# Optimization experiments

Hardware: AMD Instinct MI355X
Metric: run time of the kernel (lower is better)

Reference implementation:

```python
import jax, jax.numpy as jnp
import numpy as np

EPS = 1e-3  # tfa GroupNormalization default epsilon


def setup_inputs() -> dict:
    key = jax.random.key(0)
    ks = jax.random.split(key, 6)
    B, H, W, C = 8, 64, 64, 256
    x = jax.random.normal(ks[0], (B, H, W, C), dtype=jnp.float32)
    s = 0.05  # keep activations in a numerically sane range
    return {
        "x": x,
        "gamma": jnp.ones((C,), jnp.float32),
        "beta": jnp.zeros((C,), jnp.float32),
        "wq": jax.random.normal(ks[1], (C, C), jnp.float32) * s,
        "bq": jnp.zeros((C,), jnp.float32),
        "wk": jax.random.normal(ks[2], (C, C), jnp.float32) * s,
        "bk": jnp.zeros((C,), jnp.float32),
        "wv": jax.random.normal(ks[3], (C, C), jnp.float32) * s,
        "bv": jnp.zeros((C,), jnp.float32),
        "wp": jax.random.normal(ks[4], (C, C), jnp.float32) * s,
        "bp": jnp.zeros((C,), jnp.float32),
    }


def _group_norm1(x, gamma, beta):
    # GroupNorm with 1 group: normalize over (H, W, C) per sample,
    # per-channel affine. tfa default epsilon=1e-3.
    mean = jnp.mean(x, axis=(1, 2, 3), keepdims=True)
    var = jnp.var(x, axis=(1, 2, 3), keepdims=True)
    return (x - mean) * jax.lax.rsqrt(var + EPS) * gamma + beta


def reference(x, gamma, beta, wq, bq, wk, bk, wv, bv, wp, bp):
    B, H, W, C = x.shape
    h = _group_norm1(x, gamma, beta)
    hf = h.reshape(B, H * W, C)  # flatten spatial -> tokens
    q = hf @ wq + bq
    k = hf @ wk + bk
    v = hf @ wv + bv
    scale = jnp.float32(C) ** -0.5
    # full [B, N, N] attention scores, N = H*W (faithful to the einsum)
    scores = jnp.einsum('bnc,bmc->bnm', q, k) * scale
    attn = jax.nn.softmax(scores, axis=-1)
    o = jnp.einsum('bnm,bmc->bnc', attn, v)
    o = o @ wp + bp
    return x + o.reshape(B, H, W, C)
```

## Files before the change

### kernel.cpp

```cpp
#include <hip/hip_runtime.h>
#include <hip/hip_bf16.h>

typedef __attribute__((ext_vector_type(8))) short short8;
typedef __attribute__((ext_vector_type(4))) float f32x4;
typedef __attribute__((ext_vector_type(16))) float f32x16;
typedef long long ll_t;

#define WS_PART 0u
#define WS_WT 8192u
#define WS_ML 532480u
#define WS_Q  2097152u
#define WS_K  (WS_Q + 16777216u)
#define WS_V  (WS_K + 16777216u)
#define WS_VT (WS_V + 16777216u)
#define WS_O  (WS_VT + 16777216u)

#define SM_C2 4.3280851f

__device__ __forceinline__ unsigned short f2bf(float f) {
  unsigned int u = __builtin_bit_cast(unsigned int, f);
  u += 0x7fffu + ((u >> 16) & 1u);
  return (unsigned short)(u >> 16);
}
__device__ __forceinline__ float bf2f(unsigned short h) {
  unsigned int u = ((unsigned int)h) << 16;
  return __builtin_bit_cast(float, u);
}
__device__ __forceinline__ unsigned char f2fp8(float f) {
  return (unsigned char)(__builtin_amdgcn_cvt_pk_fp8_f32(f, f, 0, false) & 0xff);
}

__device__ __forceinline__ void gl_lds16(const unsigned short* g, unsigned short* l) {
  __builtin_amdgcn_global_load_lds(
      (const __attribute__((address_space(1))) unsigned int*)g,
      (__attribute__((address_space(3))) unsigned int*)l, 16, 0, 0);
}

__device__ __forceinline__ f32x4 mfma_fp8(ll_t a, ll_t b, f32x4 c) {
  return __builtin_amdgcn_mfma_f32_16x16x32_fp8_fp8(a, b, c, 0, 0, 0);
}

__global__ void k_wt(const float* __restrict__ wq, const float* __restrict__ wk,
                     const float* __restrict__ wv, const float* __restrict__ wp,
                     unsigned short* __restrict__ wT) {
  int m = blockIdx.x >> 8;
  int c = blockIdx.x & 255;
  const float* w = (m == 0) ? wq : (m == 1) ? wk : (m == 2) ? wv : wp;
  int d = threadIdx.x;
  wT[(size_t)(m * 256 + d) * 256 + c] = f2bf(w[c * 256 + d]);
}

__global__ void k_gn_part(const float* __restrict__ x, float2* __restrict__ part) {
  int b = blockIdx.x >> 5, seg = blockIdx.x & 31;
  const float4* xp = (const float4*)(x + ((size_t)b << 20) + ((size_t)seg << 15));
  float s = 0.f, sq = 0.f;
  for (int i = 0; i < 32; ++i) {
    float4 v = xp[threadIdx.x + i * 256];
    s += v.x + v.y + v.z + v.w;
    sq += v.x * v.x + v.y * v.y + v.z * v.z + v.w * v.w;
  }
  for (int m = 1; m <= 32; m <<= 1) { s += __shfl_xor(s, m); sq += __shfl_xor(sq, m); }
  __shared__ float2 red[4];
  int w = threadIdx.x >> 6;
  if ((threadIdx.x & 63) == 0) red[w] = make_float2(s, sq);
  __syncthreads();
  if (threadIdx.x == 0) {
    float S = 0.f, Q = 0.f;
    for (int i = 0; i < 4; ++i) { S += red[i].x; Q += red[i].y; }
    part[blockIdx.x] = make_float2(S, Q);
  }
}

__global__ __launch_bounds__(256) void k_qkv(
    const float* __restrict__ x, const float* __restrict__ gamma, const float* __restrict__ beta,
    const float* __restrict__ bq, const float* __restrict__ bk, const float* __restrict__ bv,
    const float2* __restrict__ part, const unsigned short* __restrict__ wT,
    unsigned char* __restrict__ q8, unsigned char* __restrict__ k8,
    unsigned char* __restrict__ vt8)
{
  __shared__ unsigned short SMEM[16384];
  __shared__ float2 stSh;
  unsigned short* const As = SMEM;
  unsigned short* const Bs = SMEM + 8192;
  const int bm = blockIdx.x, bn = blockIdx.y;
  const int mat = bn >> 1, dbase = (bn & 1) * 128;
  const int tid = threadIdx.x, lane = tid & 63, w = tid >> 6;
  const int wm = w >> 1, wn = w & 1;
  const int m0 = bm * 128;
  if (tid < 32) {
    float2 p = part[(bm >> 5) * 32 + tid];
    float s = p.x, sq = p.y;
    for (int m = 1; m <= 16; m <<= 1) { s += __shfl_xor(s, m); sq += __shfl_xor(sq, m); }
    if (tid == 0) {
      float mean = s * (1.f / 1048576.f);
      float var = sq * (1.f / 1048576.f) - mean * mean;
      stSh = make_float2(mean, rsqrtf(var + 1e-3f));
    }
  }
  __syncthreads();
  const float2 st = stSh;
  f32x16 acc[2][2] = {};
  for (int ks = 0; ks < 4; ++ks) {
    for (int i = 0; i < 8; ++i) {
      int chunk = tid + i * 256;
      int row = chunk >> 4, cq = (chunk & 15) * 4;
      int c = ks * 64 + cq;
      const float4 xv = *(const float4*)(x + (size_t)(m0 + row) * 256 + c);
      const float4 g = *(const float4*)(gamma + c);
      const float4 bt = *(const float4*)(beta + c);
      unsigned short h[4];
      h[0] = f2bf((xv.x - st.x) * st.y * g.x + bt.x);
      h[1] = f2bf((xv.y - st.x) * st.y * g.y + bt.y);
      h[2] = f2bf((xv.z - st.x) * st.y * g.z + bt.z);
      h[3] = f2bf((xv.w - st.x) * st.y * g.w + bt.w);
      *(uint2*)(&As[row * 64 + (cq ^ ((row & 7) << 3))]) = *(uint2*)h;
    }
    for (int i = 0; i < 4; ++i) {
      int chunk = tid + i * 256;
      int row = chunk >> 3, cc = (chunk & 7) * 8;
      const uint4* src = (const uint4*)(wT + (size_t)(mat * 256 + dbase + row) * 256 + ks * 64 + cc);
      *(uint4*)(&Bs[row * 64 + (cc ^ ((row & 7) << 3))]) = *src;
    }
    __syncthreads();
    for (int kk = 0; kk < 4; ++kk) {
      short8 a[2], b[2];
      for (int mi = 0; mi < 2; ++mi) {
        int row = wm * 64 + mi * 32 + (lane & 31);
        int off = (kk * 16 + (lane >> 5) * 8) ^ ((row & 7) << 3);
        a[mi] = *(const short8*)(&As[row * 64 + off]);
      }
      for (int ni = 0; ni < 2; ++ni) {
        int row = wn * 64 + ni * 32 + (lane & 31);
        int off = (kk * 16 + (lane >> 5) * 8) ^ ((row & 7) << 3);
        b[ni] = *(const short8*)(&Bs[row * 64 + off]);
      }
      for (int mi = 0; mi < 2; ++mi)
        for (int ni = 0; ni < 2; ++ni)
          acc[mi][ni] = __builtin_amdgcn_mfma_f32_32x32x16_bf16(a[mi], b[ni], acc[mi][ni], 0, 0, 0);
    }
    __syncthreads();
  }
  const int batch = bm >> 5;
  if (mat == 0) {
    const float qs = 0.25f * 1.44269504f;
    for (int ni = 0; ni < 2; ++ni) {
      int dcol = dbase + wn * 64 + ni * 32 + (lane & 31);
      float bv_ = bq[dcol];
      for (int mi = 0; mi < 2; ++mi)
        for (int r = 0; r < 16; ++r) {
          int rowD = (r & 3) + 8 * (r >> 2) + 4 * (lane >> 5);
          int token = m0 + wm * 64 + mi * 32 + rowD;
          q8[(size_t)token * 256 + dcol] = f2fp8((acc[mi][ni][r] + bv_) * qs);
        }
    }
  } else if (mat == 1) {
    for (int ni = 0; ni < 2; ++ni) {
      int dcol = dbase + wn * 64 + ni * 32 + (lane & 31);
      float bv_ = bk[dcol];
      size_t cbase = (size_t)(batch * 32 + (dcol >> 3)) * 32768 + (dcol & 7);
      for (int mi = 0; mi < 2; ++mi)
        for (int r = 0; r < 16; ++r) {
          int rowD = (r & 3) + 8 * (r >> 2) + 4 * (lane >> 5);
          int token = (m0 + wm * 64 + mi * 32 + rowD) & 4095;
          k8[cbase + (size_t)token * 8] = f2fp8((acc[mi][ni][r] + bv_) * 0.25f);
        }
    }
  } else {
    unsigned char* SB = (unsigned char*)SMEM;
    for (int ni = 0; ni < 2; ++ni) {
      int dloc = wn * 64 + ni * 32 + (lane & 31);
      float bv_ = bv[dbase + dloc];
      for (int mi = 0; mi < 2; ++mi)
        for (int r = 0; r < 16; ++r) {
          int tloc = wm * 64 + mi * 32 + (r & 3) + 8 * (r >> 2) + 4 * (lane >> 5);
          SB[dloc * 128 + (tloc ^ ((dloc & 7) << 4))] = f2fp8(acc[mi][ni][r] + bv_);
        }
    }
    __syncthreads();
    const int Tbase = (bm & 31) * 16;
    for (int i2 = 0; i2 < 4; ++i2) {
      int u = tid + i2 * 256;
      int T = u >> 6;
      int dp = u & 63;
      int d0 = dp * 2;
      int tb = T * 8;
      uint2 lo = *(const uint2*)(&SB[d0 * 128 + (tb ^ ((d0 & 7) << 4))]);
      uint2 hi2 = *(const uint2*)(&SB[(d0 + 1) * 128 + (tb ^ (((d0 + 1) & 7) << 4))]);
      uint4 vv = { lo.x, lo.y, hi2.x, hi2.y };
      *(uint4*)(vt8 + ((size_t)(batch * 512 + Tbase + T) * 256 + dbase + d0) * 8) = vv;
    }
  }
}

__global__ __launch_bounds__(512, 4) void k_attn(
    const unsigned char* __restrict__ q8, const unsigned char* __restrict__ k8,
    const unsigned char* __restrict__ vt8,
    unsigned short* __restrict__ part0, unsigned short* __restrict__ part1,
    float* __restrict__ lsum)
{
  __shared__ unsigned char LDSb[65536];
  unsigned char* const Ks0 = LDSb;
  unsigned char* const Ks1 = LDSb + 16384;
  unsigned char* const Vt0 = LDSb + 32768;
  unsigned char* const Vt1 = LDSb + 49152;
  const int g = blockIdx.x & 15, qt = blockIdx.x >> 4;
  const int batch = g >> 1, half = g & 1;
  const int q0 = qt * 128;
  const int tid = threadIdx.x, lane = tid & 63, li = lane & 15, hi = lane >> 4, w = tid >> 6;

  ll_t qf8[8];
  {
    const size_t qtok = (size_t)(batch * 4096 + q0 + w * 16 + li);
#pragma unroll
    for (int kt = 0; kt < 8; ++kt)
      qf8[kt] = *(const ll_t*)(q8 + qtok * 256 + kt * 32 + hi * 8);
  }
  f32x4 acc[16] = {};
  float l_r = 0.f;
  const int idx0 = ((((hi << 1) + 0) & 3) * 16 + li) << 2;
  const int idx1 = ((((hi << 1) + 1) & 3) * 16 + li) << 2;

  unsigned kSrc[2];
  int kDst[2], vOff[2];
#pragma unroll
  for (int i = 0; i < 2; ++i) {
    kSrc[i] = (unsigned)((w * 4 + 2 * i + (lane >> 5)) * 32768 + (lane & 31) * 16);
    kDst[i] = (w * 4 + 2 * i) * 512 + lane * 16;
    vOff[i] = w * 2048 + i * 1024 + lane * 16;
  }
  const unsigned char* kb = k8 + (size_t)batch * 1048576 + half * 16384;
  const unsigned char* vb = vt8 + (size_t)batch * 1048576 + half * 524288;

#define STAGE(KD, VD) do {                                              \
    _Pragma("unroll")                                                   \
    for (int i = 0; i < 2; ++i)                                         \
      gl_lds16((const unsigned short*)(kb + kSrc[i]),                   \
               (unsigned short*)(KD + kDst[i]));                        \
    _Pragma("unroll")                                                   \
    for (int i = 0; i < 2; ++i)                                         \
      gl_lds16((const unsigned short*)(vb + vOff[i]),                   \
               (unsigned short*)(VD + vOff[i]));                        \
  } while (0)

#define QK(KVF, SDST, KC) do {                                               \
    _Pragma("unroll")                                                        \
    for (int ct = 0; ct < 2; ++ct)                                           \
      _Pragma("unroll")                                                      \
      for (int kt = 0; kt < 8; ++kt) {                                       \
        int boff = (((kt * 4 + hi) * 64) + (KVF) * 32 + ct * 16 + li) * 8;   \
        ll_t kf = *(const ll_t*)(&KC[boff]);                                 \
        SDST[ct] = mfma_fp8(kf, qf8[kt], SDST[ct]);                          \
      }                                                                      \
  } while (0)

#define SOFTMAX(SARR, PF) do {                                               \
    _Pragma("unroll")                                                        \
    for (int ct = 0; ct < 2; ++ct)                                           \
      _Pragma("unroll")                                                      \
      for (int r = 0; r < 4; ++r) {                                          \
        float p = exp2f(SARR[ct][r] - SM_C2);                                \
        SARR[ct][r] = p;                                                     \
        l_r += p;                                                            \
      }                                                                      \
    int D0 = __builtin_amdgcn_cvt_pk_fp8_f32(SARR[0][0], SARR[0][1], 0, false); \
    D0 = __builtin_amdgcn_cvt_pk_fp8_f32(SARR[0][2], SARR[0][3], D0, true);     \
    int D1 = __builtin_amdgcn_cvt_pk_fp8_f32(SARR[1][0], SARR[1][1], 0, false); \
    D1 = __builtin_amdgcn_cvt_pk_fp8_f32(SARR[1][2], SARR[1][3], D1, true);     \
    int a0 = __builtin_amdgcn_ds_bpermute(idx0, D0);                         \
    int a1 = __builtin_amdgcn_ds_bpermute(idx0, D1);                         \
    int b0 = __builtin_amdgcn_ds_bpermute(idx1, D0);                         \
    int b1 = __builtin_amdgcn_ds_bpermute(idx1, D1);                         \
    bool sel = (lane & 32) != 0;                                             \
    int2 pw = { sel ? a1 : a0, sel ? b1 : b0 };                              \
    PF = __builtin_bit_cast(ll_t, pw);                                       \
  } while (0)

#define PV(KVF, PF, VC) do {                                                 \
    __builtin_amdgcn_s_setprio(1);                                          \
    _Pragma("unroll")                                                        \
    for (int dt = 0; dt < 16; ++dt) {                                        \
      int boff = ((((KVF) * 4 + hi) * 256) + dt * 16 + li) * 8;              \
      ll_t vf = *(const ll_t*)(&VC[boff]);                                   \
      acc[dt] = mfma_fp8(PF, vf, acc[dt]);                                   \
    }                                                                        \
    __builtin_amdgcn_s_setprio(0);                                          \
  } while (0)

  STAGE(Ks0, Vt0);
  for (int it = 0; it < 32; ++it) {
    const int cur = it & 1;
    __syncthreads();
    if (it < 31) {
      kb += 512;
      vb += 16384;
      if (cur) STAGE(Ks0, Vt0); else STAGE(Ks1, Vt1);
    }
    const unsigned char* Kc = cur ? Ks1 : Ks0;
    const unsigned char* Vc = cur ? Vt1 : Vt0;

    {
      f32x4 s0[2] = {};
      __builtin_amdgcn_s_setprio(1);
      QK(0, s0, Kc);
      __builtin_amdgcn_s_setprio(0);
      ll_t pf0;
      SOFTMAX(s0, pf0);
      PV(0, pf0, Vc);
    }
    {
      f32x4 s1[2] = {};
      __builtin_amdgcn_s_setprio(1);
      QK(1, s1, Kc);
      __builtin_amdgcn_s_setprio(0);
      ll_t pf1;
      SOFTMAX(s1, pf1);
      PV(1, pf1, Vc);
    }
  }
#undef STAGE
#undef QK
#undef SOFTMAX
#undef PV
  l_r += __shfl_xor(l_r, 16);
  l_r += __shfl_xor(l_r, 32);
  __syncthreads();
  if (lane < 16)
    lsum[half * 32768 + (size_t)batch * 4096 + q0 + w * 16 + lane] = l_r;
  unsigned short* Lw = (unsigned short*)LDSb + w * 4096;
#pragma unroll
  for (int dt = 0; dt < 16; ++dt)
#pragma unroll
    for (int r = 0; r < 4; ++r)
      Lw[(hi * 4 + r) * 256 + dt * 16 + li] = f2bf(acc[dt][r]);
  unsigned short* pout = (half ? part1 : part0) + ((size_t)batch * 4096 + q0 + w * 16) * 256;
#pragma unroll
  for (int i = 0; i < 8; ++i) {
    short8 v = *(const short8*)(&Lw[i * 512 + lane * 8]);
    int row = i * 2 + (lane >> 5);
    *(short8*)(pout + row * 256 + (lane & 31) * 8) = v;
  }
}

__global__ __launch_bounds__(256) void k_proj(
    const unsigned short* __restrict__ p0, const unsigned short* __restrict__ p1,
    const float* __restrict__ lsum, const unsigned short* __restrict__ wT,
    const float* __restrict__ bp, const float* __restrict__ x, float* __restrict__ out)
{
  __shared__ unsigned short As[128 * 64];
  __shared__ unsigned short Bs[128 * 64];
  const int bm = blockIdx.x, bn = blockIdx.y;
  const int dbase = bn * 128;
  const int tid = threadIdx.x, lane = tid & 63, w = tid >> 6;
  const int wm = w >> 1, wn = w & 1;
  const int m0 = bm * 128;
  f32x16 acc[2][2] = {};
  for (int ks = 0; ks < 4; ++ks) {
    for (int i = 0; i < 4; ++i) {
      int chunk = tid + i * 256;
      int row = chunk >> 3, cc = (chunk & 7) * 8;
      int tok = m0 + row;
      float r = 1.f / (lsum[tok] + lsum[32768 + tok]);
      short8 u0 = *(const short8*)(p0 + (size_t)tok * 256 + ks * 64 + cc);
      short8 u1 = *(const short8*)(p1 + (size_t)tok * 256 + ks * 64 + cc);
      unsigned short hh[8];
      for (int j = 0; j < 8; ++j)
        hh[j] = f2bf(r * (bf2f((unsigned short)u0[j]) + bf2f((unsigned short)u1[j])));
      *(uint4*)(&As[row * 64 + (cc ^ ((row & 7) << 3))]) = *(uint4*)hh;
    }
    for (int i = 0; i < 4; ++i) {
      int chunk = tid + i * 256;
      int row = chunk >> 3, cc = (chunk & 7) * 8;
      const uint4* src = (const uint4*)(wT + (size_t)(3 * 256 + dbase + row) * 256 + ks * 64 + cc);
      *(uint4*)(&Bs[row * 64 + (cc ^ ((row & 7) << 3))]) = *src;
    }
    __syncthreads();
    for (int kk = 0; kk < 4; ++kk) {
      short8 a[2], b[2];
      for (int mi = 0; mi < 2; ++mi) {
        int row = wm * 64 + mi * 32 + (lane & 31);
        int off = (kk * 16 + (lane >> 5) * 8) ^ ((row & 7) << 3);
        a[mi] = *(const short8*)(&As[row * 64 + off]);
      }
      for (int ni = 0; ni < 2; ++ni) {
        int row = wn * 64 + ni * 32 + (lane & 31);
        int off = (kk * 16 + (lane >> 5) * 8) ^ ((row & 7) << 3);
        b[ni] = *(const short8*)(&Bs[row * 64 + off]);
      }
      for (int mi = 0; mi < 2; ++mi)
        for (int ni = 0; ni < 2; ++ni)
          acc[mi][ni] = __builtin_amdgcn_mfma_f32_32x32x16_bf16(a[mi], b[ni], acc[mi][ni], 0, 0, 0);
    }
    __syncthreads();
  }
  for (int ni = 0; ni < 2; ++ni) {
    int dcol = dbase + wn * 64 + ni * 32 + (lane & 31);
    float bv_ = bp[dcol];
    for (int mi = 0; mi < 2; ++mi)
      for (int r = 0; r < 16; ++r) {
        int rowD = (r & 3) + 8 * (r >> 2) + 4 * (lane >> 5);
        size_t idx = (size_t)(m0 + wm * 64 + mi * 32 + rowD) * 256 + dcol;
        out[idx] = x[idx] + acc[mi][ni][r] + bv_;
      }
  }
}

extern "C" void kernel_launch(void* const* d_in, const int* in_sizes, int n_in,
                              void* d_out, int out_size, void* d_ws, size_t ws_size,
                              hipStream_t stream) {
  const float* x = (const float*)d_in[0];
  const float* gamma = (const float*)d_in[1];
  const float* beta = (const float*)d_in[2];
  const float* wq = (const float*)d_in[3];
  const float* bq = (const float*)d_in[4];
  const float* wk = (const float*)d_in[5];
  const float* bk = (const float*)d_in[6];
  const float* wv = (const float*)d_in[7];
  const float* bv = (const float*)d_in[8];
  const float* wp = (const float*)d_in[9];
  const float* bp = (const float*)d_in[10];
  char* ws = (char*)d_ws;
  float2* part = (float2*)(ws + WS_PART);
  unsigned short* wT = (unsigned short*)(ws + WS_WT);
  float* lsw = (float*)(ws + WS_ML);
  unsigned char* q8 = (unsigned char*)(ws + WS_Q);
  unsigned char* k8 = (unsigned char*)(ws + WS_K);
  unsigned short* vw = (unsigned short*)(ws + WS_V);
  unsigned char* vt8 = (unsigned char*)(ws + WS_VT);
  unsigned short* ow = (unsigned short*)(ws + WS_O);
  float* out = (float*)d_out;

  k_wt<<<1024, 256, 0, stream>>>(wq, wk, wv, wp, wT);
  k_gn_part<<<256, 256, 0, stream>>>(x, part);
  k_qkv<<<dim3(256, 6), 256, 0, stream>>>(x, gamma, beta, bq, bk, bv, part, wT, q8, k8, vt8);
  k_attn<<<512, 512, 0, stream>>>(q8, k8, vt8, vw, ow, lsw);
  k_proj<<<dim3(256, 2), 256, 0, stream>>>(vw, ow, lsw, wT, bp, x, out);
}
```

Before: 182.0 us.

## Merge weight transpose with GN stats; compute all QKV outputs per token tile

The weight-transpose kernel and the group-norm partial-sum kernel are merged into a single launch with block-index dispatch, removing one kernel launch. The QKV kernel is restructured so each 512-thread block normalizes a 64-token tile once into LDS and then loops over Q, K and V and both output halves. Before, each block recomputed the normalized activations for only one of six output slices, so x was read and normalized six times. The cost is more serialized per-block work, more barriers and smaller MFMA tiles per wave, which lowers parallelism (512 blocks instead of 1536).

After: 177.6 us. 1.02x faster.

```diff
diff --git a/kernel.cpp b/kernel.cpp
--- a/kernel.cpp
+++ b/kernel.cpp
@@ -40,18 +40,21 @@
   return __builtin_amdgcn_mfma_f32_16x16x32_fp8_fp8(a, b, c, 0, 0, 0);
 }
 
-__global__ void k_wt(const float* __restrict__ wq, const float* __restrict__ wk,
-                     const float* __restrict__ wv, const float* __restrict__ wp,
-                     unsigned short* __restrict__ wT) {
-  int m = blockIdx.x >> 8;
-  int c = blockIdx.x & 255;
-  const float* w = (m == 0) ? wq : (m == 1) ? wk : (m == 2) ? wv : wp;
-  int d = threadIdx.x;
-  wT[(size_t)(m * 256 + d) * 256 + c] = f2bf(w[c * 256 + d]);
-}
-
-__global__ void k_gn_part(const float* __restrict__ x, float2* __restrict__ part) {
-  int b = blockIdx.x >> 5, seg = blockIdx.x & 31;
+__global__ void k_pre(const float* __restrict__ wq, const float* __restrict__ wk,
+                      const float* __restrict__ wv, const float* __restrict__ wp,
+                      unsigned short* __restrict__ wT,
+                      const float* __restrict__ x, float2* __restrict__ part) {
+  int bid = blockIdx.x;
+  if (bid < 1024) {
+    int m = bid >> 8;
+    int c = bid & 255;
+    const float* w = (m == 0) ? wq : (m == 1) ? wk : (m == 2) ? wv : wp;
+    int d = threadIdx.x;
+    wT[(size_t)(m * 256 + d) * 256 + c] = f2bf(w[c * 256 + d]);
+    return;
+  }
+  int gb = bid - 1024;
+  int b = gb >> 5, seg = gb & 31;
   const float4* xp = (const float4*)(x + ((size_t)b << 20) + ((size_t)seg << 15));
   float s = 0.f, sq = 0.f;
   for (int i = 0; i < 32; ++i) {
@@ -67,28 +70,30 @@
   if (threadIdx.x == 0) {
     float S = 0.f, Q = 0.f;
     for (int i = 0; i < 4; ++i) { S += red[i].x; Q += red[i].y; }
-    part[blockIdx.x] = make_float2(S, Q);
-  }
-}
-
-__global__ __launch_bounds__(256) void k_qkv(
+    part[gb] = make_float2(S, Q);
+  }
+}
+
+__global__ __launch_bounds__(512) void k_qkv(
     const float* __restrict__ x, const float* __restrict__ gamma, const float* __restrict__ beta,
     const float* __restrict__ bq, const float* __restrict__ bk, const float* __restrict__ bv,
     const float2* __restrict__ part, const unsigned short* __restrict__ wT,
     unsigned char* __restrict__ q8, unsigned char* __restrict__ k8,
     unsigned char* __restrict__ vt8)
 {
-  __shared__ unsigned short SMEM[16384];
+  __shared__ unsigned char LDSQ[49152];
+  unsigned short* const As4 = (unsigned short*)LDSQ;
+  unsigned short* const Bs = (unsigned short*)(LDSQ + 32768);
+  unsigned char* const SB = LDSQ + 40960;
   __shared__ float2 stSh;
-  unsigned short* const As = SMEM;
-  unsigned short* const Bs = SMEM + 8192;
-  const int bm = blockIdx.x, bn = blockIdx.y;
-  const int mat = bn >> 1, dbase = (bn & 1) * 128;
-  const int tid = threadIdx.x, lane = tid & 63, w = tid >> 6;
-  const int wm = w >> 1, wn = w & 1;
-  const int m0 = bm * 128;
+  const int bid = blockIdx.x;
+  const int batch = bid >> 6, tile = bid & 63;
+  const int m0 = bid * 64;
+  const int tid = threadIdx.x, lane = tid & 63, l31 = lane & 31, h = lane >> 5, w = tid >> 6;
+  const int wm = w >> 2, wn = w & 3;
+
   if (tid < 32) {
-    float2 p = part[(bm >> 5) * 32 + tid];
+    float2 p = part[batch * 32 + tid];
     float s = p.x, sq = p.y;
     for (int m = 1; m <= 16; m <<= 1) { s += __shfl_xor(s, m); sq += __shfl_xor(sq, m); }
     if (tid == 0) {
@@ -99,97 +104,85 @@
   }
   __syncthreads();
   const float2 st = stSh;
-  f32x16 acc[2][2] = {};
-  for (int ks = 0; ks < 4; ++ks) {
-    for (int i = 0; i < 8; ++i) {
-      int chunk = tid + i * 256;
+
+  for (int p = 0; p < 4; ++p)
+    for (int i = 0; i < 2; ++i) {
+      int chunk = tid + i * 512;
       int row = chunk >> 4, cq = (chunk & 15) * 4;
-      int c = ks * 64 + cq;
+      int c = p * 64 + cq;
       const float4 xv = *(const float4*)(x + (size_t)(m0 + row) * 256 + c);
       const float4 g = *(const float4*)(gamma + c);
       const float4 bt = *(const float4*)(beta + c);
-      unsigned short h[4];
-      h[0] = f2bf((xv.x - st.x) * st.y * g.x + bt.x);
-      h[1] = f2bf((xv.y - st.x) * st.y * g.y + bt.y);
-      h[2] = f2bf((xv.z - st.x) * st.y * g.z + bt.z);
-      h[3] = f2bf((xv.w - st.x) * st.y * g.w + bt.w);
-      *(uint2*)(&As[row * 64 + (cq ^ ((row & 7) << 3))]) = *(uint2*)h;
-    }
-    for (int i = 0; i < 4; ++i) {
-      int chunk = tid + i * 256;
-      int row = chunk >> 3, cc = (chunk & 7) * 8;
-      const uint4* src = (const uint4*)(wT + (size_t)(mat * 256 + dbase + row) * 256 + ks * 64 + cc);
-      *(uint4*)(&Bs[row * 64 + (cc ^ ((row & 7) << 3))]) = *src;
-    }
-    __syncthreads();
-    for (int kk = 0; kk < 4; ++kk) {
-      short8 a[2], b[2];
-      for (int mi = 0; mi < 2; ++mi) {
-        int row = wm * 64 + mi * 32 + (lane & 31);
-        int off = (kk * 16 + (lane >> 5) * 8) ^ ((row & 7) << 3);
-        a[mi] = *(const short8*)(&As[row * 64 + off]);
+      unsigned short hh[4];
+      hh[0] = f2bf((xv.x - st.x) * st.y * g.x + bt.x);
+      hh[1] = f2bf((xv.y - st.x) * st.y * g.y + bt.y);
+      hh[2] = f2bf((xv.z - st.x) * st.y * g.z + bt.z);
+      hh[3] = f2bf((xv.w - st.x) * st.y * g.w + bt.w);
+      *(uint2*)(&As4[p * 4096 + row * 64 + (cq ^ ((row & 7) << 3))]) = *(uint2*)hh;
+    }
+  __syncthreads();
+
+  for (int mat = 0; mat < 3; ++mat)
+    for (int dh = 0; dh < 2; ++dh) {
+      f32x16 acc = {};
+      for (int ks = 0; ks < 4; ++ks) {
+        __syncthreads();
+        for (int i = 0; i < 2; ++i) {
+          int chunk = tid + i * 512;
+          int row = chunk >> 3, cc = (chunk & 7) * 8;
+          const uint4* src = (const uint4*)(
+              wT + (size_t)(mat * 256 + dh * 128 + row) * 256 + ks * 64 + cc);
+          *(uint4*)(&Bs[row * 64 + (cc ^ ((row & 7) << 3))]) = *src;
+        }
+        __syncthreads();
+        for (int kk = 0; kk < 4; ++kk) {
+          int rowA = wm * 32 + l31;
+          int offA = (kk * 16 + h * 8) ^ ((rowA & 7) << 3);
+          short8 a = *(const short8*)(&As4[ks * 4096 + rowA * 64 + offA]);
+          int rowB = wn * 32 + l31;
+          int offB = (kk * 16 + h * 8) ^ ((rowB & 7) << 3);
+          short8 b = *(const short8*)(&Bs[rowB * 64 + offB]);
+          acc = __builtin_amdgcn_mfma_f32_32x32x16_bf16(a, b, acc, 0, 0, 0);
+        }
       }
-      for (int ni = 0; ni < 2; ++ni) {
-        int row = wn * 64 + ni * 32 + (lane & 31);
-        int off = (kk * 16 + (lane >> 5) * 8) ^ ((row & 7) << 3);
-        b[ni] = *(const short8*)(&Bs[row * 64 + off]);
+      if (mat == 0) {
+        const float qs = 0.25f * 1.44269504f;
+        int dcol = dh * 128 + wn * 32 + l31;
+        float bv_ = bq[dcol];
+        for (int r = 0; r < 16; ++r) {
+          int rowD = (r & 3) + 8 * (r >> 2) + 4 * h;
+          int token = m0 + wm * 32 + rowD;
+          q8[(size_t)token * 256 + dcol] = f2fp8((acc[r] + bv_) * qs);
+        }
+      } else if (mat == 1) {
+        int dcol = dh * 128 + wn * 32 + l31;
+        float bv_ = bk[dcol];
+        size_t cbase = (size_t)(batch * 32 + (dcol >> 3)) * 32768 + (dcol & 7);
+        for (int r = 0; r < 16; ++r) {
+          int rowD = (r & 3) + 8 * (r >> 2) + 4 * h;
+          int token = (m0 + wm * 32 + rowD) & 4095;
+          k8[cbase + (size_t)token * 8] = f2fp8((acc[r] + bv_) * 0.25f);
+        }
+      } else {
+        int dloc = wn * 32 + l31;
+        float bv_ = bv[dh * 128 + dloc];
+        for (int r = 0; r < 16; ++r) {
+          int tloc = wm * 32 + (r & 3) + 8 * (r >> 2) + 4 * h;
+          SB[dloc * 64 + (tloc ^ ((dloc & 3) << 4))] = f2fp8(acc[r] + bv_);
+        }
+        __syncthreads();
+        {
+          int T = tid >> 6;
+          int dp = tid & 63;
+          int d0 = dp * 2;
+          int tb = T * 8;
+          uint2 lo = *(const uint2*)(&SB[d0 * 64 + (tb ^ ((d0 & 3) << 4))]);
+          uint2 hi2 = *(const uint2*)(&SB[(d0 + 1) * 64 + (tb ^ (((d0 + 1) & 3) << 4))]);
+          uint4 vv = { lo.x, lo.y, hi2.x, hi2.y };
+          *(uint4*)(vt8 + ((size_t)(batch * 512 + tile * 8 + T) * 256 + dh * 128 + d0) * 8) = vv;
+        }
       }
-      for (int mi = 0; mi < 2; ++mi)
-        for (int ni = 0; ni < 2; ++ni)
-          acc[mi][ni] = __builtin_amdgcn_mfma_f32_32x32x16_bf16(a[mi], b[ni], acc[mi][ni], 0, 0, 0);
-    }
-    __syncthreads();
-  }
-  const int batch = bm >> 5;
-  if (mat == 0) {
-    const float qs = 0.25f * 1.44269504f;
-    for (int ni = 0; ni < 2; ++ni) {
-      int dcol = dbase + wn * 64 + ni * 32 + (lane & 31);
-      float bv_ = bq[dcol];
-      for (int mi = 0; mi < 2; ++mi)
-        for (int r = 0; r < 16; ++r) {
-          int rowD = (r & 3) + 8 * (r >> 2) + 4 * (lane >> 5);
-          int token = m0 + wm * 64 + mi * 32 + rowD;
-          q8[(size_t)token * 256 + dcol] = f2fp8((acc[mi][ni][r] + bv_) * qs);
-        }
-    }
-  } else if (mat == 1) {
-    for (int ni = 0; ni < 2; ++ni) {
-      int dcol = dbase + wn * 64 + ni * 32 + (lane & 31);
-      float bv_ = bk[dcol];
-      size_t cbase = (size_t)(batch * 32 + (dcol >> 3)) * 32768 + (dcol & 7);
-      for (int mi = 0; mi < 2; ++mi)
-        for (int r = 0; r < 16; ++r) {
-          int rowD = (r & 3) + 8 * (r >> 2) + 4 * (lane >> 5);
-          int token = (m0 + wm * 64 + mi * 32 + rowD) & 4095;
-          k8[cbase + (size_t)token * 8] = f2fp8((acc[mi][ni][r] + bv_) * 0.25f);
-        }
-    }
-  } else {
-    unsigned char* SB = (unsigned char*)SMEM;
-    for (int ni = 0; ni < 2; ++ni) {
-      int dloc = wn * 64 + ni * 32 + (lane & 31);
-      float bv_ = bv[dbase + dloc];
-      for (int mi = 0; mi < 2; ++mi)
-        for (int r = 0; r < 16; ++r) {
-          int tloc = wm * 64 + mi * 32 + (r & 3) + 8 * (r >> 2) + 4 * (lane >> 5);
-          SB[dloc * 128 + (tloc ^ ((dloc & 7) << 4))] = f2fp8(acc[mi][ni][r] + bv_);
-        }
-    }
-    __syncthreads();
-    const int Tbase = (bm & 31) * 16;
-    for (int i2 = 0; i2 < 4; ++i2) {
-      int u = tid + i2 * 256;
-      int T = u >> 6;
-      int dp = u & 63;
-      int d0 = dp * 2;
-      int tb = T * 8;
-      uint2 lo = *(const uint2*)(&SB[d0 * 128 + (tb ^ ((d0 & 7) << 4))]);
-      uint2 hi2 = *(const uint2*)(&SB[(d0 + 1) * 128 + (tb ^ (((d0 + 1) & 7) << 4))]);
-      uint4 vv = { lo.x, lo.y, hi2.x, hi2.y };
-      *(uint4*)(vt8 + ((size_t)(batch * 512 + Tbase + T) * 256 + dbase + d0) * 8) = vv;
-    }
-  }
+    }
 }
 
 __global__ __launch_bounds__(512, 4) void k_attn(
@@ -429,9 +422,8 @@
   unsigned short* ow = (unsigned short*)(ws + WS_O);
   float* out = (float*)d_out;
 
-  k_wt<<<1024, 256, 0, stream>>>(wq, wk, wv, wp, wT);
-  k_gn_part<<<256, 256, 0, stream>>>(x, part);
-  k_qkv<<<dim3(256, 6), 256, 0, stream>>>(x, gamma, beta, bq, bk, bv, part, wT, q8, k8, vt8);
+  k_pre<<<1280, 256, 0, stream>>>(wq, wk, wv, wp, wT, x, part);
+  k_qkv<<<512, 512, 0, stream>>>(x, gamma, beta, bq, bk, bv, part, wT, q8, k8, vt8);
   k_attn<<<512, 512, 0, stream>>>(q8, k8, vt8, vw, ow, lsw);
   k_proj<<<dim3(256, 2), 256, 0, stream>>>(vw, ow, lsw, wT, bp, x, out);
 }
```
